# Kernel tuning notes

Hardware: AMD Instinct MI355X
Metric: run time of the kernel (lower is better)

Reference implementation:

```python
import jax, jax.numpy as jnp
import numpy as np

DT = 0.1
ROUTER_BLOCKS = 64
REPEAT = 64
IN_SIZE = 2048
HIDDEN = 4096
NNZ_W = int(IN_SIZE * HIDDEN * 0.01)   # 83886
NNZ_R = int(HIDDEN * HIDDEN * 0.01)    # 167772
BATCH = 512


def sparse_linear(x, rows, cols, vals, bias, out_features):
    """Edge-list sparse matmul: out[b, cols[e]] += x[b, rows[e]] * vals[e].
    Equivalent to torch.addmm(bias, x, W_csr) with W built from COO (coalesce
    sums duplicates; scatter-add does the same)."""
    contrib = x[:, rows] * vals  # [B, nnz]
    out = jnp.zeros((x.shape[0], out_features), x.dtype).at[:, cols].add(contrib)
    return out + bias


def setup_inputs() -> dict:
    key = jax.random.key(0)
    ks = jax.random.split(key, 20)
    inp = {}
    inp["x"] = jax.random.normal(ks[0], (BATCH, IN_SIZE), jnp.float32)
    inp["h_prev"] = jax.random.normal(ks[1], (BATCH, HIDDEN), jnp.float32)
    inp["gate"] = jax.random.uniform(ks[2], (BATCH, 1), jnp.float32)
    # SparseLinear params (init scale 1/sqrt(in_features), bias zeros)
    inp["W_vals"] = jax.random.normal(ks[3], (NNZ_W,), jnp.float32) / np.sqrt(IN_SIZE).astype(np.float32)
    inp["W_bias"] = jnp.zeros((HIDDEN,), jnp.float32)
    inp["R_vals"] = jax.random.normal(ks[4], (NNZ_R,), jnp.float32) / np.sqrt(HIDDEN).astype(np.float32)
    inp["R_bias"] = jnp.zeros((HIDDEN,), jnp.float32)
    inp["P_vals"] = jax.random.normal(ks[5], (NNZ_R,), jnp.float32) / np.sqrt(HIDDEN).astype(np.float32)
    inp["P_bias"] = jnp.zeros((HIDDEN,), jnp.float32)
    inp["router_w"] = jax.random.normal(ks[6], (ROUTER_BLOCKS, IN_SIZE), jnp.float32) / np.sqrt(IN_SIZE).astype(np.float32)
    inp["router_b"] = jnp.zeros((ROUTER_BLOCKS,), jnp.float32)
    # tau ~ U(0.1, 0.5) per TAU_CONCEPT_RANGE
    inp["tau"] = jax.random.uniform(ks[7], (HIDDEN,), jnp.float32) * 0.4 + 0.1
    # edge lists (int constants)
    inp["W_rows"] = jax.random.randint(ks[8], (NNZ_W,), 0, IN_SIZE, jnp.int32)
    inp["W_cols"] = jax.random.randint(ks[9], (NNZ_W,), 0, HIDDEN, jnp.int32)
    inp["R_rows"] = jax.random.randint(ks[10], (NNZ_R,), 0, HIDDEN, jnp.int32)
    inp["R_cols"] = jax.random.randint(ks[11], (NNZ_R,), 0, HIDDEN, jnp.int32)
    inp["P_rows"] = jax.random.randint(ks[12], (NNZ_R,), 0, HIDDEN, jnp.int32)
    inp["P_cols"] = jax.random.randint(ks[13], (NNZ_R,), 0, HIDDEN, jnp.int32)
    return inp


def reference(x, h_prev, gate, W_vals, W_bias, R_vals, R_bias, P_vals, P_bias,
              router_w, router_b, tau, W_rows, W_cols, R_rows, R_cols, P_rows, P_cols):
    r_gate = jax.nn.sigmoid(x @ router_w.T + router_b)            # [B, 64]
    mask = jnp.repeat(r_gate, REPEAT, axis=1)[:, :HIDDEN]          # [B, hidden]
    sensory = sparse_linear(x, W_rows, W_cols, W_vals, W_bias, HIDDEN) * mask
    rec = sparse_linear(h_prev, R_rows, R_cols, R_vals, R_bias, HIDDEN)
    target = jnp.tanh(sensory + rec)
    h_new = h_prev + gate * (target - h_prev) * (DT / tau)
    pred = sparse_linear(h_new, P_rows, P_cols, P_vals, P_bias, HIDDEN)
    return (h_new, pred)
```

## Files before the change

### kernel.cpp

```cpp
#include <hip/hip_runtime.h>
#include <math.h>

namespace {

constexpr int B     = 512;
constexpr int IN    = 2048;
constexpr int HID   = 4096;
constexpr int NNZ_W = 83886;
constexpr int NNZ_R = 167772;
constexpr int NTOT  = NNZ_W + 2 * NNZ_R;
constexpr int NCOLS = 3 * HID;
constexpr int SLOT  = 128;
constexpr float DT  = 0.1f;

constexpr int TRX   = 256;
constexpr int TRH   = 512;
constexpr int RTR   = 128;
constexpr int BIN   = (NTOT + 511) / 512;
constexpr int PREP2 = TRX + TRH + RTR + BIN;

typedef float f4 __attribute__((ext_vector_type(4)));
typedef float f2 __attribute__((ext_vector_type(2)));
typedef unsigned short us8 __attribute__((ext_vector_type(8)));

struct f8 { f4 lo, hi; };

__device__ __forceinline__ float bf2f(unsigned short u) {
  return __uint_as_float((unsigned int)u << 16);
}
__device__ __forceinline__ unsigned short f2bf(float f) {
  unsigned int u = __float_as_uint(f);
  u += 0x7FFFu + ((u >> 16) & 1u);
  return (unsigned short)(u >> 16);
}

__global__ void prep2_k(const float* __restrict__ x, unsigned short* __restrict__ xTb,
                        const float* __restrict__ h, float* __restrict__ hT,
                        unsigned short* __restrict__ hTb,
                        const float* __restrict__ rw, const float* __restrict__ rb,
                        float* __restrict__ rgT,
                        const int* __restrict__ Wc, const int* __restrict__ Rc,
                        const int* __restrict__ Pc, const int* __restrict__ Wr,
                        const int* __restrict__ Rr, const int* __restrict__ Pr,
                        const float* __restrict__ Wv, const float* __restrict__ Rv,
                        const float* __restrict__ Pv, int* __restrict__ cnt,
                        float2* __restrict__ packed) {
  __shared__ float sh[4 * IN];
  const int blk = blockIdx.x;
  const int tid = threadIdx.x;

  if (blk < TRX + TRH) {
    const bool isX = blk < TRX;
    const float* src; int C, tb;
    if (isX) { src = x; C = IN;  tb = blk; }
    else     { src = h; C = HID; tb = blk - TRX; }
    const int tx_n = C / 64;
    const int bx = (tb % tx_n) * 64;
    const int by = (tb / tx_n) * 64;
    const int tx = tid & 63;
    const int ty = tid >> 6;
    for (int i = ty; i < 64; i += 8)
      sh[i * 65 + tx] = src[(size_t)(by + i) * C + bx + tx];
    __syncthreads();
    for (int i = ty; i < 64; i += 8) {
      const float v = sh[tx * 65 + i];
      const size_t di = (size_t)(bx + i) * B + by + tx;
      if (isX) xTb[di] = f2bf(v);
      else     { hT[di] = v; hTb[di] = f2bf(v); }
    }
  } else if (blk < TRX + TRH + RTR) {
    const int b0 = (blk - TRX - TRH) * 4;
    for (int k = tid; k < 4 * IN; k += 512) sh[k] = x[(size_t)b0 * IN + k];
    __syncthreads();
    const int wave = tid >> 6;
    const int lane = tid & 63;
#pragma unroll
    for (int j = 0; j < 8; ++j) {
      const int o = wave * 8 + j;
      const float* w = rw + (size_t)o * IN;
      float s0 = 0.f, s1 = 0.f, s2 = 0.f, s3 = 0.f;
      for (int i = 0; i < IN / 64; ++i) {
        const float wv = w[lane + 64 * i];
        s0 += sh[0 * IN + lane + 64 * i] * wv;
        s1 += sh[1 * IN + lane + 64 * i] * wv;
        s2 += sh[2 * IN + lane + 64 * i] * wv;
        s3 += sh[3 * IN + lane + 64 * i] * wv;
      }
#pragma unroll
      for (int d = 1; d < 64; d <<= 1) {
        s0 += __shfl_xor(s0, d);
        s1 += __shfl_xor(s1, d);
        s2 += __shfl_xor(s2, d);
        s3 += __shfl_xor(s3, d);
      }
      if (lane == 0) {
        const float bias = rb[o];
        rgT[o * B + b0 + 0] = 1.f / (1.f + expf(-(s0 + bias)));
        rgT[o * B + b0 + 1] = 1.f / (1.f + expf(-(s1 + bias)));
        rgT[o * B + b0 + 2] = 1.f / (1.f + expf(-(s2 + bias)));
        rgT[o * B + b0 + 3] = 1.f / (1.f + expf(-(s3 + bias)));
      }
    }
  } else {
    const int i = (blk - TRX - TRH - RTR) * 512 + tid;
    if (i >= NTOT) return;
    int gc, r; float v;
    if (i < NNZ_W)              { gc = Wc[i];                 r = Wr[i]; v = Wv[i]; }
    else if (i < NNZ_W + NNZ_R) { int j = i - NNZ_W;          gc = HID + Rc[j];     r = Rr[j]; v = Rv[j]; }
    else                        { int j = i - NNZ_W - NNZ_R; gc = 2 * HID + Pc[j]; r = Pr[j]; v = Pv[j]; }
    const int p = atomicAdd(&cnt[gc], 1);
    packed[(size_t)gc * SLOT + p] = make_float2(v, __int_as_float(r));
  }
}

__device__ __forceinline__ f8 gather_col_bf8(const unsigned short* __restrict__ srcb,
                                             const float2* __restrict__ packed,
                                             int gc, int n, int boff, float bias) {
  f4 a0; a0.x = bias; a0.y = bias; a0.z = bias; a0.w = bias;
  f4 a1 = a0;
  const f2* ep = (const f2*)(packed + (size_t)gc * SLOT);
  int i = 0;
  for (; i + 8 <= n; i += 8) {
    f2 e[8]; us8 s[8];
#pragma unroll
    for (int j = 0; j < 8; ++j) e[j] = ep[i + j];
#pragma unroll
    for (int j = 0; j < 8; ++j)
      s[j] = *(const us8*)(srcb + (size_t)__float_as_int(e[j].y) * B + boff);
#pragma unroll
    for (int j = 0; j < 8; ++j) {
      const float v = e[j].x;
      a0.x += v * bf2f(s[j][0]); a0.y += v * bf2f(s[j][1]);
      a0.z += v * bf2f(s[j][2]); a0.w += v * bf2f(s[j][3]);
      a1.x += v * bf2f(s[j][4]); a1.y += v * bf2f(s[j][5]);
      a1.z += v * bf2f(s[j][6]); a1.w += v * bf2f(s[j][7]);
    }
  }
  for (; i < n; ++i) {
    const f2 e = ep[i];
    const us8 s = *(const us8*)(srcb + (size_t)__float_as_int(e.y) * B + boff);
    const float v = e.x;
    a0.x += v * bf2f(s[0]); a0.y += v * bf2f(s[1]);
    a0.z += v * bf2f(s[2]); a0.w += v * bf2f(s[3]);
    a1.x += v * bf2f(s[4]); a1.y += v * bf2f(s[5]);
    a1.z += v * bf2f(s[6]); a1.w += v * bf2f(s[7]);
  }
  f8 r; r.lo = a0; r.hi = a1;
  return r;
}

__device__ __forceinline__ void store_tile_T(float* __restrict__ tile,
                                             const f8 v, int wave, int lane,
                                             int c0, float* __restrict__ out) {
  ((f4*)tile)[wave * 128 + lane * 2 + 0] = v.lo;
  ((f4*)tile)[wave * 128 + lane * 2 + 1] = v.hi;
  __syncthreads();
  const int t = threadIdx.x;
#pragma unroll
  for (int r = 0; r < 2; ++r) {
    const int b = r * 256 + t;
    f4 o;
    o.x = tile[0 * 512 + b];
    o.y = tile[1 * 512 + b];
    o.z = tile[2 * 512 + b];
    o.w = tile[3 * 512 + b];
    *(f4*)(out + (size_t)b * HID + c0) = o;
  }
}

__global__ void fused_gc_k(const unsigned short* __restrict__ xTb,
                           const unsigned short* __restrict__ hTb,
                           const float* __restrict__ hT,
                           const float2* __restrict__ packed, const int* __restrict__ cnt,
                           const float* __restrict__ rgT,
                           const float* __restrict__ gate, const float* __restrict__ tau,
                           const float* __restrict__ wb, const float* __restrict__ rb,
                           float* __restrict__ out_h, unsigned short* __restrict__ hnb) {
  __shared__ float tile[4 * 512];
  const int wave = threadIdx.x >> 6, lane = threadIdx.x & 63;
  const int c0 = blockIdx.x * 4;
  const int c = c0 + wave;
  const int boff = lane * 8;

  const f8 sens = gather_col_bf8(xTb, packed, c, cnt[c], boff, wb[c]);
  const f8 rec  = gather_col_bf8(hTb, packed, HID + c, cnt[HID + c], boff, rb[c]);

  const float* rg = rgT + (size_t)(c >> 6) * B + boff;
  const f4 m0 = *(const f4*)rg;
  const f4 m1 = *(const f4*)(rg + 4);
  const f4 g0 = *(const f4*)(gate + boff);
  const f4 g1 = *(const f4*)(gate + boff + 4);
  const float* hpp = hT + (size_t)c * B + boff;
  const f4 hp0 = *(const f4*)hpp;
  const f4 hp1 = *(const f4*)(hpp + 4);
  const float k = DT / tau[c];

  f8 hn;
  hn.lo.x = hp0.x + g0.x * (tanhf(sens.lo.x * m0.x + rec.lo.x) - hp0.x) * k;
  hn.lo.y = hp0.y + g0.y * (tanhf(sens.lo.y * m0.y + rec.lo.y) - hp0.y) * k;
  hn.lo.z = hp0.z + g0.z * (tanhf(sens.lo.z * m0.z + rec.lo.z) - hp0.z) * k;
  hn.lo.w = hp0.w + g0.w * (tanhf(sens.lo.w * m0.w + rec.lo.w) - hp0.w) * k;
  hn.hi.x = hp1.x + g1.x * (tanhf(sens.hi.x * m1.x + rec.hi.x) - hp1.x) * k;
  hn.hi.y = hp1.y + g1.y * (tanhf(sens.hi.y * m1.y + rec.hi.y) - hp1.y) * k;
  hn.hi.z = hp1.z + g1.z * (tanhf(sens.hi.z * m1.z + rec.hi.z) - hp1.z) * k;
  hn.hi.w = hp1.w + g1.w * (tanhf(sens.hi.w * m1.w + rec.hi.w) - hp1.w) * k;

  us8 hb;
  hb[0] = f2bf(hn.lo.x); hb[1] = f2bf(hn.lo.y); hb[2] = f2bf(hn.lo.z); hb[3] = f2bf(hn.lo.w);
  hb[4] = f2bf(hn.hi.x); hb[5] = f2bf(hn.hi.y); hb[6] = f2bf(hn.hi.z); hb[7] = f2bf(hn.hi.w);
  *(us8*)(hnb + (size_t)c * B + boff) = hb;

  store_tile_T(tile, hn, wave, lane, c0, out_h);
}

__global__ void pred_k(const unsigned short* __restrict__ hnb,
                       const float2* __restrict__ packed, const int* __restrict__ cnt,
                       const float* __restrict__ pb, float* __restrict__ out_p) {
  __shared__ float tile[4 * 512];
  const int wave = threadIdx.x >> 6, lane = threadIdx.x & 63;
  const int c0 = blockIdx.x * 4;
  const int c = c0 + wave;
  const int boff = lane * 8;
  const f8 p = gather_col_bf8(hnb, packed, 2 * HID + c, cnt[2 * HID + c], boff, pb[c]);
  store_tile_T(tile, p, wave, lane, c0, out_p);
}

}

extern "C" void kernel_launch(void* const* d_in, const int* in_sizes, int n_in,
                              void* d_out, int out_size, void* d_ws, size_t ws_size,
                              hipStream_t stream) {
  const float* x        = (const float*)d_in[0];
  const float* h_prev   = (const float*)d_in[1];
  const float* gate     = (const float*)d_in[2];
  const float* W_vals   = (const float*)d_in[3];
  const float* W_bias   = (const float*)d_in[4];
  const float* R_vals   = (const float*)d_in[5];
  const float* R_bias   = (const float*)d_in[6];
  const float* P_vals   = (const float*)d_in[7];
  const float* P_bias   = (const float*)d_in[8];
  const float* router_w = (const float*)d_in[9];
  const float* router_b = (const float*)d_in[10];
  const float* tau      = (const float*)d_in[11];
  const int* W_rows = (const int*)d_in[12];
  const int* W_cols = (const int*)d_in[13];
  const int* R_rows = (const int*)d_in[14];
  const int* R_cols = (const int*)d_in[15];
  const int* P_rows = (const int*)d_in[16];
  const int* P_cols = (const int*)d_in[17];

  float* ws = (float*)d_ws;
  unsigned short* xTb = (unsigned short*)ws;
  float*  hT     = ws + (size_t)IN * B / 2;
  unsigned short* hTb = (unsigned short*)(hT + (size_t)HID * B);
  float*  rgT    = (float*)(hTb + (size_t)HID * B);
  unsigned short* hnb = (unsigned short*)(rgT + 64 * B);
  float2* packed = (float2*)(hnb + (size_t)HID * B);
  int*    cnt    = (int*)(packed + (size_t)NCOLS * SLOT);

  float* out_h = (float*)d_out;
  float* out_p = out_h + (size_t)B * HID;

  hipMemsetAsync(cnt, 0, NCOLS * sizeof(int), stream);

  prep2_k<<<PREP2, 512, 0, stream>>>(x, xTb, h_prev, hT, hTb,
                                     router_w, router_b, rgT,
                                     W_cols, R_cols, P_cols,
                                     W_rows, R_rows, P_rows,
                                     W_vals, R_vals, P_vals, cnt, packed);

  fused_gc_k<<<HID / 4, 256, 0, stream>>>(xTb, hTb, hT, packed, cnt, rgT,
                                          gate, tau, W_bias, R_bias, out_h, hnb);

  pred_k<<<HID / 4, 256, 0, stream>>>(hnb, packed, cnt, P_bias, out_p);
}
```

Measured before the change: 95.50 us.

## Split fused sensory/recurrent gather into separate kernels and reorder prep blocks

Splits the fused gather kernel into a sensory kernel, which writes a bf16 intermediate, and a recurrent kernel, which reads it back and applies the state update. It also reorders the prep kernel so the edge-binning blocks are scheduled first, ahead of the transpose and router blocks. The likely intent is to cut register pressure and raise occupancy in each gather kernel, and to start the atomic binning work earlier. The cost is one extra launch, an extra bf16 write and read of a 4096x512 intermediate, and rounding the sensory sum to bf16.

Result: slower. 113.0 us (+18.3%).

```diff
diff --git a/kernel.cpp b/kernel.cpp
--- a/kernel.cpp
+++ b/kernel.cpp
@@ -13,11 +13,11 @@
 constexpr int SLOT  = 128;
 constexpr float DT  = 0.1f;
 
+constexpr int BIN   = (NTOT + 511) / 512;
+constexpr int TRH   = 512;
 constexpr int TRX   = 256;
-constexpr int TRH   = 512;
 constexpr int RTR   = 128;
-constexpr int BIN   = (NTOT + 511) / 512;
-constexpr int PREP2 = TRX + TRH + RTR + BIN;
+constexpr int PREP2 = BIN + TRH + TRX + RTR;
 
 typedef float f4 __attribute__((ext_vector_type(4)));
 typedef float f2 __attribute__((ext_vector_type(2)));
@@ -49,11 +49,20 @@
   const int blk = blockIdx.x;
   const int tid = threadIdx.x;
 
-  if (blk < TRX + TRH) {
-    const bool isX = blk < TRX;
+  if (blk < BIN) {
+    const int i = blk * 512 + tid;
+    if (i >= NTOT) return;
+    int gc, r; float v;
+    if (i < NNZ_W)              { gc = Wc[i];                 r = Wr[i]; v = Wv[i]; }
+    else if (i < NNZ_W + NNZ_R) { int j = i - NNZ_W;          gc = HID + Rc[j];     r = Rr[j]; v = Rv[j]; }
+    else                        { int j = i - NNZ_W - NNZ_R; gc = 2 * HID + Pc[j]; r = Pr[j]; v = Pv[j]; }
+    const int p = atomicAdd(&cnt[gc], 1);
+    packed[(size_t)gc * SLOT + p] = make_float2(v, __int_as_float(r));
+  } else if (blk < BIN + TRH + TRX) {
+    const bool isH = blk < BIN + TRH;
     const float* src; int C, tb;
-    if (isX) { src = x; C = IN;  tb = blk; }
-    else     { src = h; C = HID; tb = blk - TRX; }
+    if (isH) { src = h; C = HID; tb = blk - BIN; }
+    else     { src = x; C = IN;  tb = blk - BIN - TRH; }
     const int tx_n = C / 64;
     const int bx = (tb % tx_n) * 64;
     const int by = (tb / tx_n) * 64;
@@ -65,11 +74,11 @@
     for (int i = ty; i < 64; i += 8) {
       const float v = sh[tx * 65 + i];
       const size_t di = (size_t)(bx + i) * B + by + tx;
-      if (isX) xTb[di] = f2bf(v);
-      else     { hT[di] = v; hTb[di] = f2bf(v); }
+      if (isH) { hT[di] = v; hTb[di] = f2bf(v); }
+      else     xTb[di] = f2bf(v);
     }
-  } else if (blk < TRX + TRH + RTR) {
-    const int b0 = (blk - TRX - TRH) * 4;
+  } else {
+    const int b0 = (blk - BIN - TRH - TRX) * 4;
     for (int k = tid; k < 4 * IN; k += 512) sh[k] = x[(size_t)b0 * IN + k];
     __syncthreads();
     const int wave = tid >> 6;
@@ -101,15 +110,6 @@
         rgT[o * B + b0 + 3] = 1.f / (1.f + expf(-(s3 + bias)));
       }
     }
-  } else {
-    const int i = (blk - TRX - TRH - RTR) * 512 + tid;
-    if (i >= NTOT) return;
-    int gc, r; float v;
-    if (i < NNZ_W)              { gc = Wc[i];                 r = Wr[i]; v = Wv[i]; }
-    else if (i < NNZ_W + NNZ_R) { int j = i - NNZ_W;          gc = HID + Rc[j];     r = Rr[j]; v = Rv[j]; }
-    else                        { int j = i - NNZ_W - NNZ_R; gc = 2 * HID + Pc[j]; r = Pr[j]; v = Pv[j]; }
-    const int p = atomicAdd(&cnt[gc], 1);
-    packed[(size_t)gc * SLOT + p] = make_float2(v, __int_as_float(r));
   }
 }
 
@@ -168,22 +168,35 @@
   }
 }
 
-__global__ void fused_gc_k(const unsigned short* __restrict__ xTb,
-                           const unsigned short* __restrict__ hTb,
-                           const float* __restrict__ hT,
-                           const float2* __restrict__ packed, const int* __restrict__ cnt,
-                           const float* __restrict__ rgT,
-                           const float* __restrict__ gate, const float* __restrict__ tau,
-                           const float* __restrict__ wb, const float* __restrict__ rb,
-                           float* __restrict__ out_h, unsigned short* __restrict__ hnb) {
+__global__ void sens_k(const unsigned short* __restrict__ xTb,
+                       const float2* __restrict__ packed, const int* __restrict__ cnt,
+                       const float* __restrict__ wb, unsigned short* __restrict__ sensb) {
+  const int wave = threadIdx.x >> 6, lane = threadIdx.x & 63;
+  const int c = blockIdx.x * 4 + wave;
+  const int boff = lane * 8;
+  const f8 s = gather_col_bf8(xTb, packed, c, cnt[c], boff, wb[c]);
+  us8 sb;
+  sb[0] = f2bf(s.lo.x); sb[1] = f2bf(s.lo.y); sb[2] = f2bf(s.lo.z); sb[3] = f2bf(s.lo.w);
+  sb[4] = f2bf(s.hi.x); sb[5] = f2bf(s.hi.y); sb[6] = f2bf(s.hi.z); sb[7] = f2bf(s.hi.w);
+  *(us8*)(sensb + (size_t)c * B + boff) = sb;
+}
+
+__global__ void rec_k(const unsigned short* __restrict__ hTb,
+                      const float* __restrict__ hT,
+                      const float2* __restrict__ packed, const int* __restrict__ cnt,
+                      const float* __restrict__ rgT,
+                      const float* __restrict__ gate, const float* __restrict__ tau,
+                      const float* __restrict__ rb,
+                      const unsigned short* __restrict__ sensb,
+                      float* __restrict__ out_h, unsigned short* __restrict__ hnb) {
   __shared__ float tile[4 * 512];
   const int wave = threadIdx.x >> 6, lane = threadIdx.x & 63;
   const int c0 = blockIdx.x * 4;
   const int c = c0 + wave;
   const int boff = lane * 8;
 
-  const f8 sens = gather_col_bf8(xTb, packed, c, cnt[c], boff, wb[c]);
-  const f8 rec  = gather_col_bf8(hTb, packed, HID + c, cnt[HID + c], boff, rb[c]);
+  const f8 rec = gather_col_bf8(hTb, packed, HID + c, cnt[HID + c], boff, rb[c]);
+  const us8 sb = *(const us8*)(sensb + (size_t)c * B + boff);
 
   const float* rg = rgT + (size_t)(c >> 6) * B + boff;
   const f4 m0 = *(const f4*)rg;
@@ -196,14 +209,14 @@
   const float k = DT / tau[c];
 
   f8 hn;
-  hn.lo.x = hp0.x + g0.x * (tanhf(sens.lo.x * m0.x + rec.lo.x) - hp0.x) * k;
-  hn.lo.y = hp0.y + g0.y * (tanhf(sens.lo.y * m0.y + rec.lo.y) - hp0.y) * k;
-  hn.lo.z = hp0.z + g0.z * (tanhf(sens.lo.z * m0.z + rec.lo.z) - hp0.z) * k;
-  hn.lo.w = hp0.w + g0.w * (tanhf(sens.lo.w * m0.w + rec.lo.w) - hp0.w) * k;
-  hn.hi.x = hp1.x + g1.x * (tanhf(sens.hi.x * m1.x + rec.hi.x) - hp1.x) * k;
-  hn.hi.y = hp1.y + g1.y * (tanhf(sens.hi.y * m1.y + rec.hi.y) - hp1.y) * k;
-  hn.hi.z = hp1.z + g1.z * (tanhf(sens.hi.z * m1.z + rec.hi.z) - hp1.z) * k;
-  hn.hi.w = hp1.w + g1.w * (tanhf(sens.hi.w * m1.w + rec.hi.w) - hp1.w) * k;
+  hn.lo.x = hp0.x + g0.x * (tanhf(bf2f(sb[0]) * m0.x + rec.lo.x) - hp0.x) * k;
+  hn.lo.y = hp0.y + g0.y * (tanhf(bf2f(sb[1]) * m0.y + rec.lo.y) - hp0.y) * k;
+  hn.lo.z = hp0.z + g0.z * (tanhf(bf2f(sb[2]) * m0.z + rec.lo.z) - hp0.z) * k;
+  hn.lo.w = hp0.w + g0.w * (tanhf(bf2f(sb[3]) * m0.w + rec.lo.w) - hp0.w) * k;
+  hn.hi.x = hp1.x + g1.x * (tanhf(bf2f(sb[4]) * m1.x + rec.hi.x) - hp1.x) * k;
+  hn.hi.y = hp1.y + g1.y * (tanhf(bf2f(sb[5]) * m1.y + rec.hi.y) - hp1.y) * k;
+  hn.hi.z = hp1.z + g1.z * (tanhf(bf2f(sb[6]) * m1.z + rec.hi.z) - hp1.z) * k;
+  hn.hi.w = hp1.w + g1.w * (tanhf(bf2f(sb[7]) * m1.w + rec.hi.w) - hp1.w) * k;
 
   us8 hb;
   hb[0] = f2bf(hn.lo.x); hb[1] = f2bf(hn.lo.y); hb[2] = f2bf(hn.lo.z); hb[3] = f2bf(hn.lo.w);
@@ -255,7 +268,8 @@
   unsigned short* hTb = (unsigned short*)(hT + (size_t)HID * B);
   float*  rgT    = (float*)(hTb + (size_t)HID * B);
   unsigned short* hnb = (unsigned short*)(rgT + 64 * B);
-  float2* packed = (float2*)(hnb + (size_t)HID * B);
+  unsigned short* sensb = hnb + (size_t)HID * B;
+  float2* packed = (float2*)(sensb + (size_t)HID * B);
   int*    cnt    = (int*)(packed + (size_t)NCOLS * SLOT);
 
   float* out_h = (float*)d_out;
@@ -269,8 +283,10 @@
                                      W_rows, R_rows, P_rows,
                                      W_vals, R_vals, P_vals, cnt, packed);
 
-  fused_gc_k<<<HID / 4, 256, 0, stream>>>(xTb, hTb, hT, packed, cnt, rgT,
-                                          gate, tau, W_bias, R_bias, out_h, hnb);
+  sens_k<<<HID / 4, 256, 0, stream>>>(xTb, packed, cnt, W_bias, sensb);
+
+  rec_k<<<HID / 4, 256, 0, stream>>>(hTb, hT, packed, cnt, rgT,
+                                     gate, tau, R_bias, sensb, out_h, hnb);
 
   pred_k<<<HID / 4, 256, 0, stream>>>(hnb, packed, cnt, P_bias, out_p);
 }
```

## Pack sparse edges as bf16 value plus 16-bit row index; batch router over 8 rows

Applied to the files above, without the earlier changes.

Each edge entry shrinks from a float2 (fp32 value plus int row) to one 32-bit word holding a bf16 weight and a 16-bit row index, which halves the bytes read per edge in the gather loops and lets eight entries load as two 128-bit vectors. The router blocks now handle 8 batch rows each, staging x as bf16 in shared memory, so half as many blocks re-read router_w. The cost is lower precision: sparse weights and router inputs are rounded to bf16, which adds numerical error, and row indices must fit in 16 bits.

New measurement: 111.7 us. 1.17x slower.

```diff
diff --git a/kernel.cpp b/kernel.cpp
--- a/kernel.cpp
+++ b/kernel.cpp
@@ -15,13 +15,13 @@
 
 constexpr int TRX   = 256;
 constexpr int TRH   = 512;
-constexpr int RTR   = 128;
+constexpr int RTR   = 64;
 constexpr int BIN   = (NTOT + 511) / 512;
 constexpr int PREP2 = TRX + TRH + RTR + BIN;
 
 typedef float f4 __attribute__((ext_vector_type(4)));
-typedef float f2 __attribute__((ext_vector_type(2)));
 typedef unsigned short us8 __attribute__((ext_vector_type(8)));
+typedef unsigned int u4 __attribute__((ext_vector_type(4)));
 
 struct f8 { f4 lo, hi; };
 
@@ -44,7 +44,7 @@
                         const int* __restrict__ Rr, const int* __restrict__ Pr,
                         const float* __restrict__ Wv, const float* __restrict__ Rv,
                         const float* __restrict__ Pv, int* __restrict__ cnt,
-                        float2* __restrict__ packed) {
+                        unsigned int* __restrict__ packed) {
   __shared__ float sh[4 * IN];
   const int blk = blockIdx.x;
   const int tid = threadIdx.x;
@@ -69,8 +69,10 @@
       else     { hT[di] = v; hTb[di] = f2bf(v); }
     }
   } else if (blk < TRX + TRH + RTR) {
-    const int b0 = (blk - TRX - TRH) * 4;
-    for (int k = tid; k < 4 * IN; k += 512) sh[k] = x[(size_t)b0 * IN + k];
+    unsigned short* shb = (unsigned short*)sh;
+    const int b0 = (blk - TRX - TRH) * 8;
+    for (int k = tid; k < 8 * IN; k += 512)
+      shb[k] = f2bf(x[(size_t)b0 * IN + k]);
     __syncthreads();
     const int wave = tid >> 6;
     const int lane = tid & 63;
@@ -78,27 +80,23 @@
     for (int j = 0; j < 8; ++j) {
       const int o = wave * 8 + j;
       const float* w = rw + (size_t)o * IN;
-      float s0 = 0.f, s1 = 0.f, s2 = 0.f, s3 = 0.f;
+      float s[8] = {0.f, 0.f, 0.f, 0.f, 0.f, 0.f, 0.f, 0.f};
       for (int i = 0; i < IN / 64; ++i) {
         const float wv = w[lane + 64 * i];
-        s0 += sh[0 * IN + lane + 64 * i] * wv;
-        s1 += sh[1 * IN + lane + 64 * i] * wv;
-        s2 += sh[2 * IN + lane + 64 * i] * wv;
-        s3 += sh[3 * IN + lane + 64 * i] * wv;
+#pragma unroll
+        for (int r = 0; r < 8; ++r)
+          s[r] += bf2f(shb[r * IN + lane + 64 * i]) * wv;
       }
 #pragma unroll
-      for (int d = 1; d < 64; d <<= 1) {
-        s0 += __shfl_xor(s0, d);
-        s1 += __shfl_xor(s1, d);
-        s2 += __shfl_xor(s2, d);
-        s3 += __shfl_xor(s3, d);
+      for (int r = 0; r < 8; ++r) {
+#pragma unroll
+        for (int d = 1; d < 64; d <<= 1) s[r] += __shfl_xor(s[r], d);
       }
       if (lane == 0) {
         const float bias = rb[o];
-        rgT[o * B + b0 + 0] = 1.f / (1.f + expf(-(s0 + bias)));
-        rgT[o * B + b0 + 1] = 1.f / (1.f + expf(-(s1 + bias)));
-        rgT[o * B + b0 + 2] = 1.f / (1.f + expf(-(s2 + bias)));
-        rgT[o * B + b0 + 3] = 1.f / (1.f + expf(-(s3 + bias)));
+#pragma unroll
+        for (int r = 0; r < 8; ++r)
+          rgT[o * B + b0 + r] = 1.f / (1.f + expf(-(s[r] + bias)));
       }
     }
   } else {
@@ -109,27 +107,28 @@
     else if (i < NNZ_W + NNZ_R) { int j = i - NNZ_W;          gc = HID + Rc[j];     r = Rr[j]; v = Rv[j]; }
     else                        { int j = i - NNZ_W - NNZ_R; gc = 2 * HID + Pc[j]; r = Pr[j]; v = Pv[j]; }
     const int p = atomicAdd(&cnt[gc], 1);
-    packed[(size_t)gc * SLOT + p] = make_float2(v, __int_as_float(r));
+    packed[(size_t)gc * SLOT + p] = ((unsigned int)f2bf(v) << 16) | (unsigned int)(r & 0xFFFF);
   }
 }
 
 __device__ __forceinline__ f8 gather_col_bf8(const unsigned short* __restrict__ srcb,
-                                             const float2* __restrict__ packed,
+                                             const unsigned int* __restrict__ packed,
                                              int gc, int n, int boff, float bias) {
   f4 a0; a0.x = bias; a0.y = bias; a0.z = bias; a0.w = bias;
   f4 a1 = a0;
-  const f2* ep = (const f2*)(packed + (size_t)gc * SLOT);
+  const unsigned int* ep = packed + (size_t)gc * SLOT;
   int i = 0;
   for (; i + 8 <= n; i += 8) {
-    f2 e[8]; us8 s[8];
-#pragma unroll
-    for (int j = 0; j < 8; ++j) e[j] = ep[i + j];
+    const u4 e0 = *(const u4*)(ep + i);
+    const u4 e1 = *(const u4*)(ep + i + 4);
+    unsigned int e[8] = {e0.x, e0.y, e0.z, e0.w, e1.x, e1.y, e1.z, e1.w};
+    us8 s[8];
 #pragma unroll
     for (int j = 0; j < 8; ++j)
-      s[j] = *(const us8*)(srcb + (size_t)__float_as_int(e[j].y) * B + boff);
+      s[j] = *(const us8*)(srcb + (size_t)(e[j] & 0xFFFFu) * B + boff);
 #pragma unroll
     for (int j = 0; j < 8; ++j) {
-      const float v = e[j].x;
+      const float v = bf2f((unsigned short)(e[j] >> 16));
       a0.x += v * bf2f(s[j][0]); a0.y += v * bf2f(s[j][1]);
       a0.z += v * bf2f(s[j][2]); a0.w += v * bf2f(s[j][3]);
       a1.x += v * bf2f(s[j][4]); a1.y += v * bf2f(s[j][5]);
@@ -137,9 +136,9 @@
     }
   }
   for (; i < n; ++i) {
-    const f2 e = ep[i];
-    const us8 s = *(const us8*)(srcb + (size_t)__float_as_int(e.y) * B + boff);
-    const float v = e.x;
+    const unsigned int e = ep[i];
+    const us8 s = *(const us8*)(srcb + (size_t)(e & 0xFFFFu) * B + boff);
+    const float v = bf2f((unsigned short)(e >> 16));
     a0.x += v * bf2f(s[0]); a0.y += v * bf2f(s[1]);
     a0.z += v * bf2f(s[2]); a0.w += v * bf2f(s[3]);
     a1.x += v * bf2f(s[4]); a1.y += v * bf2f(s[5]);
@@ -171,7 +170,7 @@
 __global__ void fused_gc_k(const unsigned short* __restrict__ xTb,
                            const unsigned short* __restrict__ hTb,
                            const float* __restrict__ hT,
-                           const float2* __restrict__ packed, const int* __restrict__ cnt,
+                           const unsigned int* __restrict__ packed, const int* __restrict__ cnt,
                            const float* __restrict__ rgT,
                            const float* __restrict__ gate, const float* __restrict__ tau,
                            const float* __restrict__ wb, const float* __restrict__ rb,
@@ -214,7 +213,7 @@
 }
 
 __global__ void pred_k(const unsigned short* __restrict__ hnb,
-                       const float2* __restrict__ packed, const int* __restrict__ cnt,
+                       const unsigned int* __restrict__ packed, const int* __restrict__ cnt,
                        const float* __restrict__ pb, float* __restrict__ out_p) {
   __shared__ float tile[4 * 512];
   const int wave = threadIdx.x >> 6, lane = threadIdx.x & 63;
@@ -255,7 +254,7 @@
   unsigned short* hTb = (unsigned short*)(hT + (size_t)HID * B);
   float*  rgT    = (float*)(hTb + (size_t)HID * B);
   unsigned short* hnb = (unsigned short*)(rgT + 64 * B);
-  float2* packed = (float2*)(hnb + (size_t)HID * B);
+  unsigned int* packed = (unsigned int*)(hnb + (size_t)HID * B);
   int*    cnt    = (int*)(packed + (size_t)NCOLS * SLOT);
 
   float* out_h = (float*)d_out;
```
